# Performance work log

Hardware: AMD Instinct MI355X
Metric: run time of the kernel (lower is better)

## Reference

```python
import jax, jax.numpy as jnp
import numpy as np

# static config matching init_kwargs
IN_SIZE = 128
OUT_SIZE = 128
KSIZE = 3
POS = 10
DIL = 1
B = 8
L = 8192


def setup_inputs() -> dict:
    key = jax.random.key(0)
    k1, k2, k3, k4, k5 = jax.random.split(key, 5)
    inputs = jax.random.normal(k1, (B, IN_SIZE, L), dtype=jnp.float32)
    connections = jax.random.randint(k2, (B, L), 0, L)  # indices into length axis
    mask = jax.random.randint(k3, (B, L), 0, 2).astype(bool)
    ch_in = (2 * IN_SIZE + POS) * KSIZE  # 798
    W = jax.random.normal(k4, (OUT_SIZE, ch_in), dtype=jnp.float32) / np.float32(np.sqrt(ch_in))
    b = jax.random.normal(k5, (OUT_SIZE,), dtype=jnp.float32) * 0.01
    return {"inputs": inputs, "connections": connections, "mask": mask, "W": W, "b": b}


def reference(inputs, connections, mask, W, b):
    Bn, C, Ln = inputs.shape
    # gather neighbor features: out[b,c,l] = inputs[b,c,connections[b,l]]  -> [B,C,L]
    conn_vals = jnp.take_along_axis(inputs, connections[:, None, :], axis=2)
    # trig positional encoding of relative offsets  -> [B,POS,L]
    pos = jnp.arange(Ln, dtype=jnp.float32)[None]              # [1,L]
    delta = (pos - connections.astype(jnp.float32))[:, None, :]  # [B,1,L]
    scales = (2.0 ** jnp.arange(POS, dtype=jnp.float32))[None, :, None]
    penc = jnp.sin(scales * delta / 1000.0)
    out = jnp.concatenate([inputs, conn_vals, penc], axis=1)   # [B, 2C+POS, L]
    # non-causal pad + unfold (window KSIZE, step 1); num windows == L
    pad = KSIZE * DIL // 2
    out = jnp.pad(out, ((0, 0), (0, 0), (pad, pad)))
    # build [B, Ch, KSIZE, L]: window k is out_padded[..., k : k+L]
    out = jnp.stack([out[..., k:k + Ln] for k in range(KSIZE)], axis=2)
    out = out.reshape(Bn, -1, Ln)                               # [B, Ch*KSIZE, L]
    # 1x1 conv == per-position GEMM
    y = jnp.einsum('oc,bcl->bol', W, out) + b[None, :, None]    # [B, OUT, L]
    return y * mask[:, None, :].astype(y.dtype)
```

## Files before the change

### kernel.cpp

```cpp
#include <hip/hip_runtime.h>
#include <math.h>

#define B_    8
#define C_    128
#define L_    8192
#define O_    128
#define POS_  10
#define CHIN  798
#define CH_   266
#define CPAD  288
#define GSTR  128
#define NCH   9
#define TL2   256
#define G_ELEMS  ((size_t)B_ * L_ * GSTR)
#define WT_ELEMS ((size_t)3 * O_ * CPAD)

typedef _Float16 half8 __attribute__((ext_vector_type(8)));
typedef short short8 __attribute__((ext_vector_type(8)));
typedef float f32x4  __attribute__((ext_vector_type(4)));

__device__ __forceinline__ void detect_core(const uint4* __restrict__ m,
                                            int* __restrict__ mflag, int tid) {
    __shared__ int s[2];
    if (tid < 2) s[tid] = 0;
    __syncthreads();
    unsigned sub = 0, mid = 0;
    #pragma unroll
    for (int k = 0; k < 16; ++k) {
        uint4 w = m[tid + k * 256];
        sub |= (w.x | w.y | w.z | w.w) & 0xFFFFFF00u;
        mid |= (w.y | w.w) & 0x000000FFu;
    }
    unsigned long long bs = __ballot(sub != 0);
    unsigned long long bm = __ballot(mid != 0);
    if ((tid & 63) == 0) {
        if (bs) atomicOr(&s[0], 1);
        if (bm) atomicOr(&s[1], 1);
    }
    __syncthreads();
    if (tid == 0) mflag[0] = s[0] ? 1 : (s[1] ? 0 : 2);
}

__global__ void detect_kernel(const uint4* __restrict__ m, int* __restrict__ mflag) {
    detect_core(m, mflag, threadIdx.x);
}

__global__ __launch_bounds__(256, 4)
void prep_kernel(const float* __restrict__ inputs, const float* __restrict__ W,
                 const uint4* __restrict__ maskv,
                 _Float16* __restrict__ G, _Float16* __restrict__ Wt,
                 int* __restrict__ mflag) {
    __shared__ float tile[64][65];
    const int bid = blockIdx.x;
    const int tid = threadIdx.x;

    if (bid == 2480) { detect_core(maskv, mflag, tid); return; }

    if (bid >= 2048) {
        int idx = (bid - 2048) * 256 + tid;
        int c   = idx % CPAD;
        int rem = idx / CPAD;
        int o   = rem & 127;
        int t   = rem >> 7;
        Wt[idx] = (c < CH_) ? (_Float16)W[o * CHIN + 3 * c + t] : (_Float16)0.f;
        return;
    }

    const int b  = bid & 7;
    const int r  = bid >> 3;
    const int c0 = (r & 1) * 64;
    const int l0 = (r >> 1) * 64;
    const int ty = tid >> 6, tx = tid & 63;

    #pragma unroll
    for (int it = 0; it < 16; ++it) {
        int cl = it * 4 + ty;
        tile[cl][tx] = inputs[((size_t)(b * C_ + c0 + cl)) * L_ + l0 + tx];
    }
    __syncthreads();
    const int cp = (tid & 31) * 2;
    const int lr = tid >> 5;
    #pragma unroll
    for (int it = 0; it < 8; ++it) {
        int ll = it * 8 + lr;
        _Float16 pair[2] = {(_Float16)tile[cp][ll], (_Float16)tile[cp + 1][ll]};
        *(unsigned*)&G[((size_t)(b * L_ + l0 + ll)) * GSTR + c0 + cp] = *(unsigned*)pair;
    }
}

__global__ __launch_bounds__(512, 1)
void k2_gemm(const _Float16* __restrict__ G, const _Float16* __restrict__ Wt,
             const int* __restrict__ conn,
             const unsigned char* __restrict__ mask,
             const float* __restrict__ bias,
             float* __restrict__ out,
             const int* __restrict__ mflag_p) {
    __shared__ _Float16 As[3][128][40];
    __shared__ _Float16 Bs[260][40];
    __shared__ int conn_s[260];

    const int bid = blockIdx.x;
    const int b   = bid & 7;
    const int l0  = (bid >> 3) * TL2;
    const int tid  = threadIdx.x;
    const int wave = tid >> 6;
    const int lane = tid & 63;
    const int wo = wave & 1;
    const int wl = wave >> 1;
    const int g  = lane >> 4;
    const int ln = lane & 15;

    const _Float16* gb = G + (size_t)b * L_ * GSTR;

    for (int j = tid; j < TL2 + 2; j += 512) {
        int l_ = l0 - 1 + j;
        conn_s[j] = ((unsigned)l_ < (unsigned)L_) ? conn[b * L_ + l_] : 0;
    }

    auto aload = [&](int ch, int q) -> short8 {
        int cb = q & 3, o = (q >> 2) & 127, tp = q >> 9;
        return *(const short8*)&Wt[((size_t)(tp * O_ + o)) * CPAD + ch * 32 + cb * 8];
    };
    auto bload = [&](int ch, int q) -> short8 {
        int cb = q & 3, j = q >> 2;
        int l_ = l0 - 1 + j;
        short8 v = (short8)0;
        if ((unsigned)l_ < (unsigned)L_) {
            if (ch < 4) {
                v = *(const short8*)&gb[(size_t)l_ * GSTR + ch * 32 + cb * 8];
            } else if (ch < 8) {
                int cj = conn_s[j];
                v = *(const short8*)&gb[(size_t)cj * GSTR + (ch - 4) * 32 + cb * 8];
            } else if (cb < 2) {
                float d = (float)(l_ - conn_s[j]);
                _Float16 h[8];
                #pragma unroll
                for (int e = 0; e < 8; ++e) {
                    int p = cb * 8 + e;
                    h[e] = (p < POS_) ? (_Float16)sinf(((float)(1 << p)) * d / 1000.0f)
                                      : (_Float16)0.f;
                }
                v = *(short8*)h;
            }
        }
        return v;
    };
    auto awrite = [&](short8 s, int q) {
        int cb = q & 3, o = (q >> 2) & 127, tp = q >> 9;
        *(short8*)&As[tp][o][cb * 8] = s;
    };
    auto bwrite = [&](short8 s, int q) {
        int cb = q & 3, j = q >> 2;
        *(short8*)&Bs[j][cb * 8] = s;
    };

    f32x4 acc[4][4];
    #pragma unroll
    for (int m = 0; m < 4; ++m)
        #pragma unroll
        for (int n = 0; n < 4; ++n) acc[m][n] = (f32x4)0.f;

    {
        short8 a0 = aload(0, tid), a1 = aload(0, tid + 512), a2 = aload(0, tid + 1024);
        short8 s0 = bload(0, tid), s1 = bload(0, tid + 512);
        short8 s2; if (tid < 8) s2 = bload(0, 1024 + tid);
        awrite(a0, tid); awrite(a1, tid + 512); awrite(a2, tid + 1024);
        bwrite(s0, tid); bwrite(s1, tid + 512);
        if (tid < 8) bwrite(s2, 1024 + tid);
    }
    __syncthreads();

    for (int ch = 0; ch < NCH; ++ch) {
        const bool more = (ch + 1 < NCH);

        short8 a0, a1, a2, s0, s1, s2;
        if (more) {
            a0 = aload(ch + 1, tid); a1 = aload(ch + 1, tid + 512); a2 = aload(ch + 1, tid + 1024);
            s0 = bload(ch + 1, tid); s1 = bload(ch + 1, tid + 512);
            if (tid < 8) s2 = bload(ch + 1, 1024 + tid);
        }

        #pragma unroll
        for (int t = 0; t < 3; ++t) {
            half8 bf[4];
            #pragma unroll
            for (int n = 0; n < 4; ++n)
                bf[n] = *(const half8*)&Bs[wl * 64 + n * 16 + ln + t][8 * g];
            #pragma unroll
            for (int m = 0; m < 4; ++m) {
                half8 af = *(const half8*)&As[t][wo * 64 + m * 16 + ln][8 * g];
                #pragma unroll
                for (int n = 0; n < 4; ++n)
                    acc[m][n] = __builtin_amdgcn_mfma_f32_16x16x32_f16(af, bf[n], acc[m][n], 0, 0, 0);
            }
        }

        if (more) {
            __syncthreads();
            awrite(a0, tid); awrite(a1, tid + 512); awrite(a2, tid + 1024);
            bwrite(s0, tid); bwrite(s1, tid + 512);
            if (tid < 8) bwrite(s2, 1024 + tid);
            __syncthreads();
        }
    }

    const int mflag = mflag_p[0];
    float mv[4];
    #pragma unroll
    for (int n = 0; n < 4; ++n) {
        int l = l0 + wl * 64 + n * 16 + ln;
        int idx = b * L_ + l;
        if (mflag == 1)      mv[n] = mask[idx] ? 1.f : 0.f;
        else if (mflag == 0) mv[n] = ((const int*)mask)[idx] ? 1.f : 0.f;
        else                 mv[n] = ((const int*)mask)[2 * idx] ? 1.f : 0.f;
    }
    #pragma unroll
    for (int m = 0; m < 4; ++m) {
        #pragma unroll
        for (int r = 0; r < 4; ++r) {
            int o = wo * 64 + m * 16 + g * 4 + r;
            float bo = bias[o];
            #pragma unroll
            for (int n = 0; n < 4; ++n) {
                int l = l0 + wl * 64 + n * 16 + ln;
                out[((size_t)(b * O_ + o)) * L_ + l] = (acc[m][n][r] + bo) * mv[n];
            }
        }
    }
}

__global__ __launch_bounds__(256, 2)
void cc_fallback_kernel(const float* __restrict__ inputs,
                        const int* __restrict__ conn,
                        const unsigned char* __restrict__ mask,
                        const float* __restrict__ W,
                        const float* __restrict__ bias,
                        float* __restrict__ out,
                        const int* __restrict__ mflag_p) {
    __shared__ int   conn_s[130];
    __shared__ float feat_s[16][132];
    __shared__ float Ws[48][136];

    const int b   = blockIdx.y;
    const int l0  = blockIdx.x * 128;
    const int tid = threadIdx.x;
    const int ot  = tid >> 4;
    const int lt  = tid & 15;
    const int o0  = ot * 8;
    const int ll  = lt * 8;

    for (int j = tid; j < 130; j += 256) {
        int lg = l0 - 1 + j;
        conn_s[j] = ((unsigned)lg < (unsigned)L_) ? conn[b * L_ + lg] : -1;
    }
    float acc[8][8];
    #pragma unroll
    for (int i = 0; i < 8; ++i)
        #pragma unroll
        for (int j = 0; j < 8; ++j) acc[i][j] = 0.f;

    const int tc = ot, tj = lt;
    for (int chunk = 0; chunk < 17; ++chunk) {
        const int CN  = (chunk < 16) ? 16 : POS_;
        const int cg0 = chunk * 16;
        const int col0 = 3 * cg0;
        __syncthreads();
        {
            const int nw = O_ * CN * 3;
            for (int idx = tid; idx < nw; idx += 256) {
                int o = idx & 127, kk = idx >> 7;
                Ws[kk][o] = W[o * CHIN + col0 + kk];
            }
        }
        if (chunk < 8) {
            const float* src = inputs + ((size_t)b * C_ + (cg0 + tc)) * L_;
            for (int j = tj; j < 130; j += 16) {
                int lg = l0 - 1 + j;
                feat_s[tc][j] = ((unsigned)lg < (unsigned)L_) ? src[lg] : 0.f;
            }
        } else if (chunk < 16) {
            const float* src = inputs + ((size_t)b * C_ + (cg0 - 128 + tc)) * L_;
            for (int j = tj; j < 130; j += 16) {
                int cj = conn_s[j];
                feat_s[tc][j] = (cj >= 0) ? src[cj] : 0.f;
            }
        } else if (tc < POS_) {
            const float sc = (float)(1 << tc);
            for (int j = tj; j < 130; j += 16) {
                int cj = conn_s[j];
                int lg = l0 - 1 + j;
                float v = 0.f;
                if (cj >= 0) v = sinf((sc * (float)(lg - cj)) / 1000.0f);
                feat_s[tc][j] = v;
            }
        }
        __syncthreads();
        for (int c = 0; c < CN; ++c) {
            float f[10];
            float4 fa = *(const float4*)&feat_s[c][ll];
            float4 fb = *(const float4*)&feat_s[c][ll + 4];
            float2 fc2 = *(const float2*)&feat_s[c][ll + 8];
            f[0]=fa.x; f[1]=fa.y; f[2]=fa.z; f[3]=fa.w;
            f[4]=fb.x; f[5]=fb.y; f[6]=fb.z; f[7]=fb.w;
            f[8]=fc2.x; f[9]=fc2.y;
            #pragma unroll
            for (int k = 0; k < 3; ++k) {
                const float* wrow = &Ws[c * 3 + k][o0];
                float4 wa = *(const float4*)&wrow[0];
                float4 wb = *(const float4*)&wrow[4];
                float w[8] = {wa.x, wa.y, wa.z, wa.w, wb.x, wb.y, wb.z, wb.w};
                #pragma unroll
                for (int oi = 0; oi < 8; ++oi)
                    #pragma unroll
                    for (int li = 0; li < 8; ++li)
                        acc[oi][li] = fmaf(w[oi], f[li + k], acc[oi][li]);
            }
        }
    }
    const int mflag = mflag_p[0];
    const int lbase = l0 + ll;
    float mv[8];
    #pragma unroll
    for (int li = 0; li < 8; ++li) {
        int idx = b * L_ + lbase + li;
        if (mflag == 1)      mv[li] = mask[idx] ? 1.f : 0.f;
        else if (mflag == 0) mv[li] = ((const int*)mask)[idx] ? 1.f : 0.f;
        else                 mv[li] = ((const int*)mask)[2 * idx] ? 1.f : 0.f;
    }
    #pragma unroll
    for (int oi = 0; oi < 8; ++oi) {
        float bo = bias[o0 + oi];
        float* dst = out + ((size_t)b * O_ + o0 + oi) * L_ + lbase;
        #pragma unroll
        for (int li = 0; li < 8; ++li) dst[li] = (acc[oi][li] + bo) * mv[li];
    }
}

extern "C" void kernel_launch(void* const* d_in, const int* in_sizes, int n_in,
                              void* d_out, int out_size, void* d_ws, size_t ws_size,
                              hipStream_t stream) {
    const float*         inputs = (const float*)d_in[0];
    const int*           conn   = (const int*)d_in[1];
    const unsigned char* mask   = (const unsigned char*)d_in[2];
    const float*         W      = (const float*)d_in[3];
    const float*         bias   = (const float*)d_in[4];
    float*               out    = (float*)d_out;

    const size_t g_bytes  = G_ELEMS * sizeof(_Float16);
    const size_t wt_bytes = WT_ELEMS * sizeof(_Float16);
    const size_t need     = g_bytes + wt_bytes + 64;

    if (ws_size < need) {
        int* mflag = (int*)d_ws;
        detect_kernel<<<1, 256, 0, stream>>>((const uint4*)mask, mflag);
        dim3 grid(L_ / 128, B_);
        cc_fallback_kernel<<<grid, 256, 0, stream>>>(inputs, conn, mask, W, bias, out, mflag);
        return;
    }

    _Float16* G     = (_Float16*)d_ws;
    _Float16* Wt    = (_Float16*)((char*)d_ws + g_bytes);
    int*      mflag = (int*)((char*)d_ws + g_bytes + wt_bytes);

    prep_kernel<<<2481, 256, 0, stream>>>(inputs, W, (const uint4*)mask, G, Wt, mflag);
    k2_gemm<<<256, 512, 0, stream>>>(G, Wt, conn, mask, bias, out, mflag);
}
```

Before: 46.91 us.

## Load weights directly to registers and give each wave a private B tile

The GEMM kernel no longer stages the weight tiles in shared memory. Each wave loads its MFMA A fragments straight from a chunk-major repacked weight buffer into registers, and the prep kernel now builds that buffer. Each wave also keeps its own 66-row B tile in LDS and double-buffers it through registers, so all block-wide __syncthreads inside the channel loop go away. The cost is many more registers (two A fragment sets plus two B sets) under a launch bound of 2 blocks per CU, redundant global weight reads across waves, and halo rows reloaded per wave.

```diff
diff --git a/kernel.cpp b/kernel.cpp
--- a/kernel.cpp
+++ b/kernel.cpp
@@ -8,12 +8,11 @@
 #define POS_  10
 #define CHIN  798
 #define CH_   266
-#define CPAD  288
 #define GSTR  128
 #define NCH   9
 #define TL2   256
 #define G_ELEMS  ((size_t)B_ * L_ * GSTR)
-#define WT_ELEMS ((size_t)3 * O_ * CPAD)
+#define WT_ELEMS ((size_t)3 * NCH * O_ * 32)
 
 typedef _Float16 half8 __attribute__((ext_vector_type(8)));
 typedef short short8 __attribute__((ext_vector_type(8)));
@@ -48,7 +47,7 @@
 __global__ __launch_bounds__(256, 4)
 void prep_kernel(const float* __restrict__ inputs, const float* __restrict__ W,
                  const uint4* __restrict__ maskv,
-                 _Float16* __restrict__ G, _Float16* __restrict__ Wt,
+                 _Float16* __restrict__ G, _Float16* __restrict__ Wt2,
                  int* __restrict__ mflag) {
     __shared__ float tile[64][65];
     const int bid = blockIdx.x;
@@ -58,11 +57,13 @@
 
     if (bid >= 2048) {
         int idx = (bid - 2048) * 256 + tid;
-        int c   = idx % CPAD;
-        int rem = idx / CPAD;
-        int o   = rem & 127;
-        int t   = rem >> 7;
-        Wt[idx] = (c < CH_) ? (_Float16)W[o * CHIN + 3 * c + t] : (_Float16)0.f;
+        int cc  = idx & 31;
+        int o   = (idx >> 5) & 127;
+        int tch = idx >> 12;
+        int ch  = tch % 9;
+        int t   = tch / 9;
+        int cg  = ch * 32 + cc;
+        Wt2[idx] = (cg < CH_) ? (_Float16)W[o * CHIN + 3 * cg + t] : (_Float16)0.f;
         return;
     }
 
@@ -88,16 +89,15 @@
     }
 }
 
-__global__ __launch_bounds__(512, 1)
-void k2_gemm(const _Float16* __restrict__ G, const _Float16* __restrict__ Wt,
+__global__ __launch_bounds__(512, 2)
+void k2_gemm(const _Float16* __restrict__ G, const _Float16* __restrict__ Wt2,
              const int* __restrict__ conn,
              const unsigned char* __restrict__ mask,
              const float* __restrict__ bias,
              float* __restrict__ out,
              const int* __restrict__ mflag_p) {
-    __shared__ _Float16 As[3][128][40];
-    __shared__ _Float16 Bs[260][40];
-    __shared__ int conn_s[260];
+    __shared__ _Float16 Bs[8][66][40];
+    __shared__ int conn_s[258];
 
     const int bid = blockIdx.x;
     const int b   = bid & 7;
@@ -109,30 +109,29 @@
     const int wl = wave >> 1;
     const int g  = lane >> 4;
     const int ln = lane & 15;
+    const int lw0 = l0 + wl * 64 - 1;
 
     const _Float16* gb = G + (size_t)b * L_ * GSTR;
+    _Float16 (*bsw)[40] = Bs[wave];
 
     for (int j = tid; j < TL2 + 2; j += 512) {
         int l_ = l0 - 1 + j;
         conn_s[j] = ((unsigned)l_ < (unsigned)L_) ? conn[b * L_ + l_] : 0;
     }
-
-    auto aload = [&](int ch, int q) -> short8 {
-        int cb = q & 3, o = (q >> 2) & 127, tp = q >> 9;
-        return *(const short8*)&Wt[((size_t)(tp * O_ + o)) * CPAD + ch * 32 + cb * 8];
-    };
-    auto bload = [&](int ch, int q) -> short8 {
+    __syncthreads();
+
+    auto bload = [&](int ch, int q) -> half8 {
         int cb = q & 3, j = q >> 2;
-        int l_ = l0 - 1 + j;
-        short8 v = (short8)0;
+        int l_ = lw0 + j;
+        half8 v = (half8)0;
         if ((unsigned)l_ < (unsigned)L_) {
             if (ch < 4) {
-                v = *(const short8*)&gb[(size_t)l_ * GSTR + ch * 32 + cb * 8];
+                v = *(const half8*)&gb[(size_t)l_ * GSTR + ch * 32 + cb * 8];
             } else if (ch < 8) {
-                int cj = conn_s[j];
-                v = *(const short8*)&gb[(size_t)cj * GSTR + (ch - 4) * 32 + cb * 8];
+                int cj = conn_s[wl * 64 + j];
+                v = *(const half8*)&gb[(size_t)cj * GSTR + (ch - 4) * 32 + cb * 8];
             } else if (cb < 2) {
-                float d = (float)(l_ - conn_s[j]);
+                float d = (float)(l_ - conn_s[wl * 64 + j]);
                 _Float16 h[8];
                 #pragma unroll
                 for (int e = 0; e < 8; ++e) {
@@ -140,19 +139,31 @@
                     h[e] = (p < POS_) ? (_Float16)sinf(((float)(1 << p)) * d / 1000.0f)
                                       : (_Float16)0.f;
                 }
-                v = *(short8*)h;
+                v = *(half8*)h;
             }
         }
         return v;
     };
-    auto awrite = [&](short8 s, int q) {
-        int cb = q & 3, o = (q >> 2) & 127, tp = q >> 9;
-        *(short8*)&As[tp][o][cb * 8] = s;
-    };
-    auto bwrite = [&](short8 s, int q) {
-        int cb = q & 3, j = q >> 2;
-        *(short8*)&Bs[j][cb * 8] = s;
-    };
+
+#define ALOADF(DST, CH) { _Pragma("unroll") for (int t_ = 0; t_ < 3; ++t_) \
+        _Pragma("unroll") for (int m_ = 0; m_ < 4; ++m_) \
+            DST[t_][m_] = *(const half8*)&Wt2[((size_t)((t_ * NCH + (CH)) * O_ + wo * 64 + m_ * 16 + ln)) * 32 + g * 8]; }
+
+#define BLOADF(DST, CH) { _Pragma("unroll") for (int it_ = 0; it_ < 5; ++it_) { \
+        int q_ = it_ * 64 + lane; \
+        DST[it_] = (q_ < 264) ? bload((CH), q_) : (half8)0; } }
+
+#define BWRITEF(SRC) { _Pragma("unroll") for (int it_ = 0; it_ < 5; ++it_) { \
+        int q_ = it_ * 64 + lane; \
+        if (q_ < 264) { int cb_ = q_ & 3, j_ = q_ >> 2; *(half8*)&bsw[j_][cb_ * 8] = SRC[it_]; } } }
+
+#define COMPUTE(AUSE) { _Pragma("unroll") for (int t_ = 0; t_ < 3; ++t_) { \
+        half8 bf_[4]; \
+        _Pragma("unroll") for (int n_ = 0; n_ < 4; ++n_) \
+            bf_[n_] = *(const half8*)&bsw[n_ * 16 + ln + t_][8 * g]; \
+        _Pragma("unroll") for (int m_ = 0; m_ < 4; ++m_) \
+            _Pragma("unroll") for (int n_ = 0; n_ < 4; ++n_) \
+                acc[m_][n_] = __builtin_amdgcn_mfma_f32_16x16x32_f16(AUSE[t_][m_], bf_[n_], acc[m_][n_], 0, 0, 0); } }
 
     f32x4 acc[4][4];
     #pragma unroll
@@ -160,47 +171,18 @@
         #pragma unroll
         for (int n = 0; n < 4; ++n) acc[m][n] = (f32x4)0.f;
 
-    {
-        short8 a0 = aload(0, tid), a1 = aload(0, tid + 512), a2 = aload(0, tid + 1024);
-        short8 s0 = bload(0, tid), s1 = bload(0, tid + 512);
-        short8 s2; if (tid < 8) s2 = bload(0, 1024 + tid);
-        awrite(a0, tid); awrite(a1, tid + 512); awrite(a2, tid + 1024);
-        bwrite(s0, tid); bwrite(s1, tid + 512);
-        if (tid < 8) bwrite(s2, 1024 + tid);
-    }
-    __syncthreads();
-
-    for (int ch = 0; ch < NCH; ++ch) {
-        const bool more = (ch + 1 < NCH);
-
-        short8 a0, a1, a2, s0, s1, s2;
-        if (more) {
-            a0 = aload(ch + 1, tid); a1 = aload(ch + 1, tid + 512); a2 = aload(ch + 1, tid + 1024);
-            s0 = bload(ch + 1, tid); s1 = bload(ch + 1, tid + 512);
-            if (tid < 8) s2 = bload(ch + 1, 1024 + tid);
-        }
-
-        #pragma unroll
-        for (int t = 0; t < 3; ++t) {
-            half8 bf[4];
-            #pragma unroll
-            for (int n = 0; n < 4; ++n)
-                bf[n] = *(const half8*)&Bs[wl * 64 + n * 16 + ln + t][8 * g];
-            #pragma unroll
-            for (int m = 0; m < 4; ++m) {
-                half8 af = *(const half8*)&As[t][wo * 64 + m * 16 + ln][8 * g];
-                #pragma unroll
-                for (int n = 0; n < 4; ++n)
-                    acc[m][n] = __builtin_amdgcn_mfma_f32_16x16x32_f16(af, bf[n], acc[m][n], 0, 0, 0);
-            }
-        }
-
-        if (more) {
-            __syncthreads();
-            awrite(a0, tid); awrite(a1, tid + 512); awrite(a2, tid + 1024);
-            bwrite(s0, tid); bwrite(s1, tid + 512);
-            if (tid < 8) bwrite(s2, 1024 + tid);
-            __syncthreads();
+    half8 A0[3][4], A1[3][4], B0[5], B1[5];
+    ALOADF(A0, 0);
+    BLOADF(B0, 0);
+
+    for (int ch = 0; ch < NCH; ch += 2) {
+        BWRITEF(B0);
+        if (ch + 1 < NCH) { ALOADF(A1, ch + 1); BLOADF(B1, ch + 1); }
+        COMPUTE(A0);
+        if (ch + 1 < NCH) {
+            BWRITEF(B1);
+            if (ch + 2 < NCH) { ALOADF(A0, ch + 2); BLOADF(B0, ch + 2); }
+            COMPUTE(A1);
         }
     }
 
@@ -227,6 +209,10 @@
             }
         }
     }
+#undef ALOADF
+#undef BLOADF
+#undef BWRITEF
+#undef COMPUTE
 }
 
 __global__ __launch_bounds__(256, 2)
@@ -359,9 +345,9 @@
     }
 
     _Float16* G     = (_Float16*)d_ws;
-    _Float16* Wt    = (_Float16*)((char*)d_ws + g_bytes);
+    _Float16* Wt2   = (_Float16*)((char*)d_ws + g_bytes);
     int*      mflag = (int*)((char*)d_ws + g_bytes + wt_bytes);
 
-    prep_kernel<<<2481, 256, 0, stream>>>(inputs, W, (const uint4*)mask, G, Wt, mflag);
-    k2_gemm<<<256, 512, 0, stream>>>(G, Wt, conn, mask, bias, out, mflag);
-}
+    prep_kernel<<<2481, 256, 0, stream>>>(inputs, W, (const uint4*)mask, G, Wt2, mflag);
+    k2_gemm<<<256, 512, 0, stream>>>(G, Wt2, conn, mask, bias, out, mflag);
+}
```

Measured after the change: 52.89 us. 12.8% more time.
